# Performance work log

Measured on AMD Instinct MI355X. Metric: run time of the kernel, lower is better.

Reference implementation:

```python
import jax, jax.numpy as jnp
import numpy as np

B, T, E, H = 4, 8192, 1024, 16
D = E // H
SCALE = 1.0 / np.sqrt(D).astype(np.float32)
EPS_FM = 1e-6
EPS_Z = 1e-8


def setup_inputs() -> dict:
    key = jax.random.key(0)
    ks = jax.random.split(key, 11)
    s = 1.0 / np.sqrt(E).astype(np.float32)  # small init so feature map stays sane
    return {
        'query': jax.random.normal(ks[0], (B, T, E), jnp.float32),
        'key': jax.random.normal(ks[1], (B, T, E), jnp.float32),
        'value': jax.random.normal(ks[2], (B, T, E), jnp.float32),
        'Wq': jax.random.normal(ks[3], (E, E), jnp.float32) * s,
        'bq': jax.random.normal(ks[4], (E,), jnp.float32) * 0.01,
        'Wk': jax.random.normal(ks[5], (E, E), jnp.float32) * s,
        'bk': jax.random.normal(ks[6], (E,), jnp.float32) * 0.01,
        'Wv': jax.random.normal(ks[7], (E, E), jnp.float32) * s,
        'bv': jax.random.normal(ks[8], (E,), jnp.float32) * 0.01,
        'Wo': jax.random.normal(ks[9], (E, E), jnp.float32) * s,
        'bo': jax.random.normal(ks[10], (E,), jnp.float32) * 0.01,
    }


def _heads(x):
    # (B, T, E) -> (B, H, T, D)
    b, t, _ = x.shape
    return x.reshape(b, t, H, D).transpose(0, 2, 1, 3)


def _feature_map(x):
    return jax.nn.relu(x) + EPS_FM


def reference(query, key, value, Wq, bq, Wk, bk, Wv, bv, Wo, bo):
    b, tq, _ = query.shape
    Q = _feature_map(_heads(query @ Wq.T + bq) * SCALE)  # (B,H,Tq,D)
    K = _feature_map(_heads(key @ Wk.T + bk) * SCALE)    # (B,H,Tk,D)
    V = _heads(value @ Wv.T + bv)                         # (B,H,Tk,D)
    KV = jnp.einsum('bhnd,bhne->bhde', K, V)              # (B,H,D,D)
    K_sum = K.sum(axis=2)                                 # (B,H,D)
    Z = jnp.einsum('bhnd,bhd->bhn', Q, K_sum) + EPS_Z     # (B,H,Tq)
    out = jnp.einsum('bhnd,bhde->bhne', Q, KV) / Z[..., None]
    out = out.transpose(0, 2, 1, 3).reshape(b, tq, E)
    return out @ Wo.T + bo
```

## Files before the change

kernel.cpp:

```cpp
#include <hip/hip_runtime.h>
#include <hip/hip_bf16.h>


#define SCALE_ 0.125f
#define EPS_FM_ 1e-6f
#define EPS_Z_ 1e-8f

typedef __bf16 bf16;
typedef __attribute__((ext_vector_type(4))) __bf16 bf16x4;
typedef __attribute__((ext_vector_type(8))) __bf16 bf16x8;
typedef __attribute__((ext_vector_type(8))) unsigned short u16x8;
typedef __attribute__((ext_vector_type(4))) float f32x4;

__device__ __forceinline__ void gl_lds16(const void* g, void* l) {
  __builtin_amdgcn_global_load_lds(
      (const __attribute__((address_space(1))) void*)g,
      (__attribute__((address_space(3))) void*)l, 16, 0, 0);
}

#define SBAR()                                  \
  do {                                          \
    __builtin_amdgcn_sched_barrier(0);          \
    asm volatile("s_barrier" ::: "memory");     \
    __builtin_amdgcn_sched_barrier(0);          \
  } while (0)

__global__ __launch_bounds__(256) void cast_weights(
    const float* __restrict__ Wq, const float* __restrict__ Wk,
    const float* __restrict__ Wv, const float* __restrict__ Wo,
    bf16* __restrict__ out) {
  int which = blockIdx.y;
  int j = (blockIdx.x * 256 + threadIdx.x) * 4;
  const float* s = (which == 0) ? Wq : (which == 1) ? Wk : (which == 2) ? Wv : Wo;
  float4 v = *(const float4*)(s + j);
  bf16x4 p = {(bf16)v.x, (bf16)v.y, (bf16)v.z, (bf16)v.w};
  *(bf16x4*)(out + (size_t)which * (1u << 20) + j) = p;
}

template <int MODE>
__global__ __launch_bounds__(512, 2) void gemm8p(
    const bf16* __restrict__ Ab, const float* __restrict__ Aq,
    const float* __restrict__ Ak, const float* __restrict__ Av,
    const bf16* __restrict__ Wb, const float* __restrict__ b0,
    const float* __restrict__ b1, const float* __restrict__ b2,
    bf16* __restrict__ Pb, float* __restrict__ Pf) {
  __shared__ __align__(16) char lds[65536];
  const int tid = threadIdx.x;
  const int bid = blockIdx.x;
  const int wg = (bid & 7) * (gridDim.x >> 3) + (bid >> 3);
  const int mt = wg >> 2;
  int seg = 0, om = 2;
  if constexpr (MODE == 0) {
    seg = mt >> 7;
    om = (seg < 2) ? 0 : 1;
  }
  const int m0 = (MODE == 0 ? (mt & 127) : mt) * 256;
  const int n0 = (wg & 3) * 256;
  const int wave = tid >> 6, lane = tid & 63;
  const int wm = wave >> 2, wn = wave & 3;
  const int l16 = lane & 15, kg = lane >> 4;
  const int e = l16 & 7;
  const int sw0 = (kg ^ e) << 4;
  const int sw1 = ((4 | kg) ^ e) << 4;

  const int tr = tid >> 3;
  const int cslot = (tid & 7) ^ (tr & 7);
  const bf16* pA = nullptr;
  const float* pAf = nullptr;
  if constexpr (MODE == 1)
    pA = Ab + (size_t)(m0 + tr) * 1024 + cslot * 8;
  else {
    const float* Af = (seg == 0) ? Aq : (seg == 1) ? Ak : Av;
    pAf = Af + (size_t)(m0 + tr) * 1024 + cslot * 8;
  }
  const bf16* W = (MODE == 0) ? Wb + ((size_t)seg << 20) : Wb;
  const float* bias = (MODE == 0) ? ((seg == 0) ? b0 : (seg == 1) ? b1 : b2) : b0;
  const bf16* pB = W + (size_t)(n0 + ((tr >> 5) << 6) + (tr & 31)) * 1024 + cslot * 8;
  char* sA = lds;
  char* sB = lds + 32768;

  auto stgA = [&](int h, int kt) {
    const bf16* g = pA + h * 65536 + kt * 64;
    char* d = sA + h * 16384 + tid * 16;
    gl_lds16(g, d);
    gl_lds16(g + 131072, d + 8192);
  };
  auto stgB = [&](int h, int kt) {
    const bf16* g = pB + h * 32768 + kt * 64;
    char* d = sB + h * 16384 + tid * 16;
    gl_lds16(g, d);
    gl_lds16(g + 131072, d + 8192);
  };
  auto ldgA = [&](int h, int kt, f32x4* r) {
    const float* g = pAf + h * 65536 + kt * 64;
    r[0] = *(const f32x4*)g;
    r[1] = *(const f32x4*)(g + 4);
    r[2] = *(const f32x4*)(g + 131072);
    r[3] = *(const f32x4*)(g + 131072 + 4);
  };
  auto wrA = [&](int h, const f32x4* r) {
    bf16x8 p0 = {(bf16)r[0][0], (bf16)r[0][1], (bf16)r[0][2], (bf16)r[0][3],
                 (bf16)r[1][0], (bf16)r[1][1], (bf16)r[1][2], (bf16)r[1][3]};
    bf16x8 p1 = {(bf16)r[2][0], (bf16)r[2][1], (bf16)r[2][2], (bf16)r[2][3],
                 (bf16)r[3][0], (bf16)r[3][1], (bf16)r[3][2], (bf16)r[3][3]};
    char* d = sA + h * 16384 + tid * 16;
    *(bf16x8*)d = p0;
    *(bf16x8*)(d + 8192) = p1;
  };

  const int aBase = wm * 8192 + l16 * 128;
  const int bBase = wn * 4096 + l16 * 128;
  auto ldA = [&](int h, int fmi, int kk) {
    return *(const bf16x8*)(sA + h * 16384 + aBase + fmi * 2048 +
                            (kk ? sw1 : sw0));
  };
  auto ldB = [&](int h, int fnj, int kk) {
    return *(const bf16x8*)(sB + h * 16384 + bBase + fnj * 2048 +
                            (kk ? sw1 : sw0));
  };

  f32x4 acc[8][4] = {};
  bf16x8 rA[4][2], rB01[2][2], rB23[2][2];
  f32x4 ga[4], gb[4];
  const int NT = 16;

  if constexpr (MODE == 1) {
    stgA(0, 0); stgB(0, 0); stgB(1, 0); stgA(1, 0);
    asm volatile("s_waitcnt vmcnt(2)" ::: "memory");
  } else {
    ldgA(0, 0, ga); ldgA(1, 0, gb);
    stgB(0, 0); stgB(1, 0);
    asm volatile("s_waitcnt vmcnt(12)" ::: "memory");
    wrA(0, ga);
    asm volatile("s_waitcnt vmcnt(4)" ::: "memory");
    wrA(1, gb);
    ldgA(0, 1, ga); ldgA(1, 1, gb);
    asm volatile("s_waitcnt vmcnt(8)" ::: "memory");
    asm volatile("s_waitcnt lgkmcnt(0)" ::: "memory");
  }
  SBAR();

#pragma unroll 2
  for (int t = 0; t < NT; ++t) {
#pragma unroll
    for (int fmi = 0; fmi < 4; ++fmi) {
      rA[fmi][0] = ldA(0, fmi, 0);
      rA[fmi][1] = ldA(0, fmi, 1);
    }
#pragma unroll
    for (int fnj = 0; fnj < 2; ++fnj) {
      rB01[fnj][0] = ldB(0, fnj, 0);
      rB01[fnj][1] = ldB(0, fnj, 1);
    }
    SBAR();
    __builtin_amdgcn_s_setprio(1);
#pragma unroll
    for (int fmi = 0; fmi < 4; ++fmi)
#pragma unroll
      for (int fnj = 0; fnj < 2; ++fnj)
#pragma unroll
        for (int kk = 0; kk < 2; ++kk)
          acc[fmi][fnj] = __builtin_amdgcn_mfma_f32_16x16x32_bf16(
              rA[fmi][kk], rB01[fnj][kk], acc[fmi][fnj], 0, 0, 0);
    __builtin_amdgcn_s_setprio(0);
    SBAR();
#pragma unroll
    for (int fnj = 0; fnj < 2; ++fnj) {
      rB23[fnj][0] = ldB(1, fnj, 0);
      rB23[fnj][1] = ldB(1, fnj, 1);
    }
    if (t + 1 < NT) {
      if constexpr (MODE == 1) stgA(0, t + 1);
      stgB(0, t + 1);
    }
    SBAR();
    __builtin_amdgcn_s_setprio(1);
#pragma unroll
    for (int fmi = 0; fmi < 4; ++fmi)
#pragma unroll
      for (int fnj = 0; fnj < 2; ++fnj)
#pragma unroll
        for (int kk = 0; kk < 2; ++kk)
          acc[fmi][2 + fnj] = __builtin_amdgcn_mfma_f32_16x16x32_bf16(
              rA[fmi][kk], rB23[fnj][kk], acc[fmi][2 + fnj], 0, 0, 0);
    __builtin_amdgcn_s_setprio(0);
    __builtin_amdgcn_sched_barrier(0);
    if constexpr (MODE == 1) {
      if (t + 1 < NT)
        asm volatile("s_waitcnt vmcnt(4)" ::: "memory");
      else
        asm volatile("s_waitcnt vmcnt(0)" ::: "memory");
    }
    SBAR();
#pragma unroll
    for (int fmi = 0; fmi < 4; ++fmi) {
      rA[fmi][0] = ldA(1, fmi, 0);
      rA[fmi][1] = ldA(1, fmi, 1);
    }
    if (t + 1 < NT) stgB(1, t + 1);
    SBAR();
    __builtin_amdgcn_s_setprio(1);
#pragma unroll
    for (int fmi = 0; fmi < 4; ++fmi)
#pragma unroll
      for (int fnj = 0; fnj < 2; ++fnj)
#pragma unroll
        for (int kk = 0; kk < 2; ++kk)
          acc[4 + fmi][2 + fnj] = __builtin_amdgcn_mfma_f32_16x16x32_bf16(
              rA[fmi][kk], rB23[fnj][kk], acc[4 + fmi][2 + fnj], 0, 0, 0);
    __builtin_amdgcn_s_setprio(0);
    __builtin_amdgcn_sched_barrier(0);
    if constexpr (MODE == 0) {
      if (t + 1 < NT) {
        wrA(0, ga);
        if (t + 2 < NT) ldgA(0, t + 2, ga);
      }
    }
    SBAR();
    if constexpr (MODE == 1) {
      if (t + 1 < NT) stgA(1, t + 1);
    }
    SBAR();
    __builtin_amdgcn_s_setprio(1);
#pragma unroll
    for (int fmi = 0; fmi < 4; ++fmi)
#pragma unroll
      for (int fnj = 0; fnj < 2; ++fnj)
#pragma unroll
        for (int kk = 0; kk < 2; ++kk)
          acc[4 + fmi][fnj] = __builtin_amdgcn_mfma_f32_16x16x32_bf16(
              rA[fmi][kk], rB01[fnj][kk], acc[4 + fmi][fnj], 0, 0, 0);
    __builtin_amdgcn_s_setprio(0);
    __builtin_amdgcn_sched_barrier(0);
    if constexpr (MODE == 0) {
      if (t + 1 < NT) {
        wrA(1, gb);
        if (t + 2 < NT) {
          ldgA(1, t + 2, gb);
          asm volatile("s_waitcnt vmcnt(8)" ::: "memory");
        } else {
          asm volatile("s_waitcnt vmcnt(0)" ::: "memory");
        }
      }
    } else {
      if (t + 1 < NT)
        asm volatile("s_waitcnt vmcnt(2)" ::: "memory");
    }
    SBAR();
  }

  if constexpr (MODE == 0) {
    bf16* PbS = Pb + (size_t)seg * 33554432u;
#pragma unroll
    for (int hk = 0; hk < 2; ++hk) {
      if (wm == hk) {
#pragma unroll
        for (int fn = 0; fn < 4; ++fn) {
          const int col = wn * 64 + fn * 16 + l16;
          const float bv = bias[n0 + col];
#pragma unroll
          for (int fm = 0; fm < 8; ++fm) {
            const int rl0 = fm * 16 + kg * 4;
#pragma unroll
            for (int i = 0; i < 4; ++i) {
              float v = acc[fm][fn][i] + bv;
              if (om == 0) { v *= SCALE_; v = fmaxf(v, 0.f) + EPS_FM_; }
              const int rl = rl0 + i;
              bf16 bvv = (bf16)v;
              *(unsigned short*)(lds + rl * 512 + ((((col >> 3) ^ (rl & 7))) << 4) +
                                 (col & 7) * 2) =
                  __builtin_bit_cast(unsigned short, bvv);
            }
          }
        }
      }
      __syncthreads();
#pragma unroll
      for (int it = 0; it < 8; ++it) {
        const int gi = it * 512 + tid;
        const int row = gi >> 5, g = gi & 31;
        bf16x8 v = *(const bf16x8*)(lds + row * 512 + ((g ^ (row & 7)) << 4));
        *(bf16x8*)(PbS + (size_t)(m0 + hk * 128 + row) * 1024 + n0 + g * 8) = v;
      }
      __syncthreads();
    }
  } else {
#pragma unroll
    for (int fn = 0; fn < 4; ++fn) {
      const int col = n0 + wn * 64 + fn * 16 + l16;
      const float bv = bias[col];
#pragma unroll
      for (int fm = 0; fm < 8; ++fm) {
        const int row = m0 + wm * 128 + fm * 16 + kg * 4;
#pragma unroll
        for (int i = 0; i < 4; ++i)
          Pf[(size_t)(row + i) * 1024 + col] = acc[fm][fn][i] + bv;
      }
    }
  }
}

__global__ __launch_bounds__(256) void kv_mfma(
    const bf16* __restrict__ Kp, const bf16* __restrict__ Vp,
    float* __restrict__ KVpart, float* __restrict__ KsumPart) {
  __shared__ __align__(16) char lds[65536];
  char* Kt = lds;
  char* Vt = lds + 32768;
  const int bh = blockIdx.x, split = blockIdx.y;
  const int b = bh >> 4, h = bh & 15;
  const int tid = threadIdx.x;
  const int p = tid >> 3, c = tid & 7;
  const int wave = tid >> 6, lane = tid & 63;
  const int wd = wave >> 1, we = wave & 1;
  const int l16 = lane & 15, kg = lane >> 4;
  f32x4 acc[2][2] = {};
  f32x4 accz[2] = {};
  const bf16x8 ones = {1.f, 1.f, 1.f, 1.f, 1.f, 1.f, 1.f, 1.f};
  const size_t gbase0 =
      (size_t)(b * 8192 + split * 1024) * 1024 + h * 64 + c * 8;

  bf16x8 pk0[4], pk1[4], pv0[4], pv1[4];
#pragma unroll
  for (int i = 0; i < 4; ++i) {
    const size_t ga = gbase0 + (size_t)(i * 64 + p * 2) * 1024;
    pk0[i] = *(const bf16x8*)(Kp + ga);
    pk1[i] = *(const bf16x8*)(Kp + ga + 1024);
    pv0[i] = *(const bf16x8*)(Vp + ga);
    pv1[i] = *(const bf16x8*)(Vp + ga + 1024);
  }

  for (int o = 0; o < 4; ++o) {
    __syncthreads();
#pragma unroll
    for (int i = 0; i < 4; ++i) {
      const int t = i * 64 + p * 2;
      u16x8 a0 = __builtin_bit_cast(u16x8, pk0[i]);
      u16x8 a1 = __builtin_bit_cast(u16x8, pk1[i]);
      u16x8 b0 = __builtin_bit_cast(u16x8, pv0[i]);
      u16x8 b1 = __builtin_bit_cast(u16x8, pv1[i]);
      const int gt = t >> 3, tl = (t & 7) * 2;
#pragma unroll
      for (int j = 0; j < 8; ++j) {
        const int d = c * 8 + j;
        const int off = d * 512 + ((gt ^ (d & 7) ^ c) << 4) + tl;
        *(unsigned int*)(Kt + off) =
            (unsigned int)a0[j] | ((unsigned int)a1[j] << 16);
        *(unsigned int*)(Vt + off) =
            (unsigned int)b0[j] | ((unsigned int)b1[j] << 16);
      }
    }
    __syncthreads();
    if (o + 1 < 4) {
#pragma unroll
      for (int i = 0; i < 4; ++i) {
        const size_t ga = gbase0 + (size_t)((o + 1) * 256 + i * 64 + p * 2) * 1024;
        pk0[i] = *(const bf16x8*)(Kp + ga);
        pk1[i] = *(const bf16x8*)(Kp + ga + 1024);
        pv0[i] = *(const bf16x8*)(Vp + ga);
        pv1[i] = *(const bf16x8*)(Vp + ga + 1024);
      }
    }

#pragma unroll
    for (int ks = 0; ks < 8; ++ks) {
      const int g = ks * 4 + kg;
      bf16x8 af[2], bf_[2];
#pragma unroll
      for (int f = 0; f < 2; ++f) {
        const int d = wd * 32 + f * 16 + l16;
        af[f] = *(const bf16x8*)(Kt + d * 512 +
                                 ((g ^ (d & 7) ^ ((d >> 3) & 7)) << 4));
        const int ee = we * 32 + f * 16 + l16;
        bf_[f] = *(const bf16x8*)(Vt + ee * 512 +
                                  ((g ^ (ee & 7) ^ ((ee >> 3) & 7)) << 4));
      }
#pragma unroll
      for (int fa = 0; fa < 2; ++fa) {
#pragma unroll
        for (int fb = 0; fb < 2; ++fb)
          acc[fa][fb] = __builtin_amdgcn_mfma_f32_16x16x32_bf16(
              af[fa], bf_[fb], acc[fa][fb], 0, 0, 0);
        if (we == 0)
          accz[fa] = __builtin_amdgcn_mfma_f32_16x16x32_bf16(
              af[fa], ones, accz[fa], 0, 0, 0);
      }
    }
  }

  float* outp = KVpart + ((size_t)split * 64 + bh) * 4096;
#pragma unroll
  for (int fa = 0; fa < 2; ++fa)
#pragma unroll
    for (int i = 0; i < 4; ++i) {
      const int d = wd * 32 + fa * 16 + kg * 4 + i;
#pragma unroll
      for (int fb = 0; fb < 2; ++fb)
        outp[d * 64 + we * 32 + fb * 16 + l16] = acc[fa][fb][i];
      if (we == 0 && l16 == 0)
        KsumPart[((size_t)split * 64 + bh) * 64 + d] = accz[fa][i];
    }
}

__global__ __launch_bounds__(256) void kv_reduce(
    const float* __restrict__ KVpart, const float* __restrict__ KsumPart,
    bf16* __restrict__ KVt) {
  int bh = blockIdx.x >> 2;
  int q = blockIdx.x & 3;
  for (int idx = q * 1280 + threadIdx.x; idx < (q + 1) * 1280; idx += 256) {
    float s = 0.f;
    if (idx < 4096) {
      int e = idx >> 6, d = idx & 63;
      for (int sp = 0; sp < 8; ++sp)
        s += KVpart[((size_t)sp * 64 + bh) * 4096 + d * 64 + e];
    } else if (idx < 4160) {
      int d = idx - 4096;
      for (int sp = 0; sp < 8; ++sp)
        s += KsumPart[((size_t)sp * 64 + bh) * 64 + d];
    }
    KVt[(size_t)bh * 5120 + idx] = (bf16)s;
  }
}

__global__ __launch_bounds__(256) void attn(
    const bf16* __restrict__ KVt, bf16* __restrict__ QA) {
  __shared__ __align__(16) char lds[43008];
  char* Qt = lds;
  char* Bt = lds + 32768;
  const int bh = blockIdx.x, tc = blockIdx.y;
  const int b = bh >> 4, h = bh & 15;
  const int tid = threadIdx.x;
  const int m0 = b * 8192 + tc * 256;

#pragma unroll
  for (int i = 0; i < 8; ++i) {
    const int gidx = i * 256 + tid;
    const int row = gidx >> 3, g = gidx & 7;
    const int gsrc = g ^ (row & 7);
    gl_lds16(QA + (size_t)(m0 + row) * 1024 + h * 64 + gsrc * 8, Qt + gidx * 16);
  }
#pragma unroll
  for (int i = 0; i < 3; ++i) {
    const int gidx = i * 256 + tid;
    if (gidx < 640) {
      const int row = gidx >> 3, g = gidx & 7;
      const int gsrc = g ^ (row & 7);
      gl_lds16(KVt + (size_t)bh * 5120 + row * 64 + gsrc * 8, Bt + gidx * 16);
    }
  }
  __syncthreads();

  const int wave = tid >> 6, lane = tid & 63;
  const int l16 = lane & 15, kg = lane >> 4;
  bf16x8 a[4][2];
#pragma unroll
  for (int fm = 0; fm < 4; ++fm)
#pragma unroll
    for (int kk = 0; kk < 2; ++kk) {
      const int row = wave * 64 + fm * 16 + l16;
      const int g = kk * 4 + kg;
      a[fm][kk] = *(const bf16x8*)(Qt + row * 128 + ((g ^ (row & 7)) << 4));
    }
  f32x4 acc[4][4] = {};
  f32x4 accz[4] = {};
#pragma unroll
  for (int kk = 0; kk < 2; ++kk) {
    const int g = kk * 4 + kg;
    const int zr = 64 + l16;
    bf16x8 bz = *(const bf16x8*)(Bt + zr * 128 + ((g ^ (zr & 7)) << 4));
#pragma unroll
    for (int fn = 0; fn < 4; ++fn) {
      const int br = fn * 16 + l16;
      bf16x8 bb = *(const bf16x8*)(Bt + br * 128 + ((g ^ (br & 7)) << 4));
#pragma unroll
      for (int fm = 0; fm < 4; ++fm)
        acc[fm][fn] = __builtin_amdgcn_mfma_f32_16x16x32_bf16(
            a[fm][kk], bb, acc[fm][fn], 0, 0, 0);
    }
#pragma unroll
    for (int fm = 0; fm < 4; ++fm)
      accz[fm] = __builtin_amdgcn_mfma_f32_16x16x32_bf16(
          a[fm][kk], bz, accz[fm], 0, 0, 0);
  }
  __syncthreads();

#pragma unroll
  for (int fm = 0; fm < 4; ++fm)
#pragma unroll
    for (int i = 0; i < 4; ++i) {
      const float z = __shfl(accz[fm][i], (lane & 48), 64) + EPS_Z_;
      const float rz = 1.0f / z;
      const int row = wave * 64 + fm * 16 + kg * 4 + i;
#pragma unroll
      for (int fn = 0; fn < 4; ++fn) {
        const int col = fn * 16 + l16;
        const int gc = col >> 3;
        bf16 v = (bf16)(acc[fm][fn][i] * rz);
        *(unsigned short*)(Qt + row * 128 + ((gc ^ (row & 7)) << 4) + (col & 7) * 2) =
            __builtin_bit_cast(unsigned short, v);
      }
    }
  __syncthreads();

#pragma unroll
  for (int i = 0; i < 8; ++i) {
    const int gidx = i * 256 + tid;
    const int row = gidx >> 3, g = gidx & 7;
    bf16x8 v = *(const bf16x8*)(Qt + row * 128 + ((g ^ (row & 7)) << 4));
    *(bf16x8*)(QA + (size_t)(m0 + row) * 1024 + h * 64 + g * 8) = v;
  }
}

extern "C" void kernel_launch(void* const* d_in, const int* in_sizes, int n_in,
                              void* d_out, int out_size, void* d_ws, size_t ws_size,
                              hipStream_t stream) {
  const float* query = (const float*)d_in[0];
  const float* key = (const float*)d_in[1];
  const float* value = (const float*)d_in[2];
  const float* Wq = (const float*)d_in[3];
  const float* bq = (const float*)d_in[4];
  const float* Wk = (const float*)d_in[5];
  const float* bk = (const float*)d_in[6];
  const float* Wv = (const float*)d_in[7];
  const float* bv = (const float*)d_in[8];
  const float* Wo = (const float*)d_in[9];
  const float* bo = (const float*)d_in[10];
  float* out = (float*)d_out;

  bf16* ws = (bf16*)d_ws;
  bf16* Wqb = ws;
  bf16* Wob = ws + (3u << 20);
  bf16* Qp = ws + (4u << 20);
  bf16* Kp = Qp + 33554432u;
  bf16* Vp = Kp + 33554432u;
  bf16* KVt = Vp + 33554432u;
  float* KVpart = (float*)d_out + 16777216u;
  float* KsumPart = KVpart + 8 * 64 * 4096;

  cast_weights<<<dim3(1024, 4), 256, 0, stream>>>(Wq, Wk, Wv, Wo, Wqb);

  gemm8p<0><<<1536, 512, 0, stream>>>(nullptr, query, key, value, Wqb, bq, bk,
                                      bv, Qp, nullptr);

  kv_mfma<<<dim3(64, 8), 256, 0, stream>>>(Kp, Vp, KVpart, KsumPart);
  kv_reduce<<<256, 256, 0, stream>>>(KVpart, KsumPart, KVt);
  attn<<<dim3(64, 32), 256, 0, stream>>>(KVt, Qp);
  gemm8p<1><<<512, 512, 0, stream>>>(Qp, nullptr, nullptr, nullptr, Wob, bo,
                                     bo, bo, nullptr, out);
}
```

Before: 428.1 us.

## Double-buffer B weight tiles in LDS for the fused QKV projection GEMM

For the QKV projection GEMM (MODE 0), the B (weight) tile gets a second LDS buffer. The next k-step's B tile is issued at the start of each iteration into the alternate buffer, instead of being staged piecewise mid-iteration. This is meant to hide weight-load latency behind more MFMA work. LDS use grows from 64KB to 96KB for this mode, which may prevent two 512-thread blocks from fitting per CU. The changed vmcnt waits in the unseen part of the loop must also stay consistent with the extra outstanding loads.

```diff
diff --git a/kernel.cpp b/kernel.cpp
--- a/kernel.cpp
+++ b/kernel.cpp
@@ -44,7 +44,7 @@
     const bf16* __restrict__ Wb, const float* __restrict__ b0,
     const float* __restrict__ b1, const float* __restrict__ b2,
     bf16* __restrict__ Pb, float* __restrict__ Pf) {
-  __shared__ __align__(16) char lds[65536];
+  __shared__ __align__(16) char lds[MODE == 0 ? 98304 : 65536];
   const int tid = threadIdx.x;
   const int bid = blockIdx.x;
   const int wg = (bid & 7) * (gridDim.x >> 3) + (bid >> 3);
@@ -85,9 +85,9 @@
     gl_lds16(g, d);
     gl_lds16(g + 131072, d + 8192);
   };
-  auto stgB = [&](int h, int kt) {
+  auto stgB = [&](int h, int kt, int bb) {
     const bf16* g = pB + h * 32768 + kt * 64;
-    char* d = sB + h * 16384 + tid * 16;
+    char* d = sB + bb * 32768 + h * 16384 + tid * 16;
     gl_lds16(g, d);
     gl_lds16(g + 131072, d + 8192);
   };
@@ -114,8 +114,8 @@
     return *(const bf16x8*)(sA + h * 16384 + aBase + fmi * 2048 +
                             (kk ? sw1 : sw0));
   };
-  auto ldB = [&](int h, int fnj, int kk) {
-    return *(const bf16x8*)(sB + h * 16384 + bBase + fnj * 2048 +
+  auto ldB = [&](int bb, int h, int fnj, int kk) {
+    return *(const bf16x8*)(sB + bb * 32768 + h * 16384 + bBase + fnj * 2048 +
                             (kk ? sw1 : sw0));
   };
 
@@ -125,23 +125,25 @@
   const int NT = 16;
 
   if constexpr (MODE == 1) {
-    stgA(0, 0); stgB(0, 0); stgB(1, 0); stgA(1, 0);
+    stgA(0, 0); stgB(0, 0, 0); stgB(1, 0, 0); stgA(1, 0);
     asm volatile("s_waitcnt vmcnt(2)" ::: "memory");
   } else {
     ldgA(0, 0, ga); ldgA(1, 0, gb);
-    stgB(0, 0); stgB(1, 0);
+    stgB(0, 0, 0); stgB(1, 0, 0);
+    stgB(0, 1, 1); stgB(1, 1, 1);
     asm volatile("s_waitcnt vmcnt(12)" ::: "memory");
     wrA(0, ga);
-    asm volatile("s_waitcnt vmcnt(4)" ::: "memory");
+    asm volatile("s_waitcnt vmcnt(8)" ::: "memory");
     wrA(1, gb);
     ldgA(0, 1, ga); ldgA(1, 1, gb);
-    asm volatile("s_waitcnt vmcnt(8)" ::: "memory");
+    asm volatile("s_waitcnt vmcnt(12)" ::: "memory");
     asm volatile("s_waitcnt lgkmcnt(0)" ::: "memory");
   }
   SBAR();
 
 #pragma unroll 2
   for (int t = 0; t < NT; ++t) {
+    const int c = t & 1;
 #pragma unroll
     for (int fmi = 0; fmi < 4; ++fmi) {
       rA[fmi][0] = ldA(0, fmi, 0);
@@ -149,8 +151,14 @@
     }
 #pragma unroll
     for (int fnj = 0; fnj < 2; ++fnj) {
-      rB01[fnj][0] = ldB(0, fnj, 0);
-      rB01[fnj][1] = ldB(0, fnj, 1);
+      rB01[fnj][0] = ldB(MODE == 0 ? c : 0, 0, fnj, 0);
+      rB01[fnj][1] = ldB(MODE == 0 ? c : 0, 0, fnj, 1);
+    }
+    if constexpr (MODE == 0) {
+      if (t + 1 < NT) {
+        stgB(0, t + 1, c ^ 1);
+        stgB(1, t + 1, c ^ 1);
+      }
     }
     SBAR();
     __builtin_amdgcn_s_setprio(1);
@@ -166,12 +174,14 @@
     SBAR();
 #pragma unroll
     for (int fnj = 0; fnj < 2; ++fnj) {
-      rB23[fnj][0] = ldB(1, fnj, 0);
-      rB23[fnj][1] = ldB(1, fnj, 1);
-    }
-    if (t + 1 < NT) {
-      if constexpr (MODE == 1) stgA(0, t + 1);
-      stgB(0, t + 1);
+      rB23[fnj][0] = ldB(MODE == 0 ? c : 0, 1, fnj, 0);
+      rB23[fnj][1] = ldB(MODE == 0 ? c : 0, 1, fnj, 1);
+    }
+    if constexpr (MODE == 1) {
+      if (t + 1 < NT) {
+        stgA(0, t + 1);
+        stgB(0, t + 1, 0);
+      }
     }
     SBAR();
     __builtin_amdgcn_s_setprio(1);
@@ -197,7 +207,9 @@
       rA[fmi][0] = ldA(1, fmi, 0);
       rA[fmi][1] = ldA(1, fmi, 1);
     }
-    if (t + 1 < NT) stgB(1, t + 1);
+    if constexpr (MODE == 1) {
+      if (t + 1 < NT) stgB(1, t + 1, 0);
+    }
     SBAR();
     __builtin_amdgcn_s_setprio(1);
 #pragma unroll
```

New measurement: 452.2 us. 5.6% more time.
